# Kernel tuning notes

Measured on AMD Instinct MI355X. Metric: run time of the kernel, lower is better.

## Reference

```python
import jax, jax.numpy as jnp
import numpy as np

TAU, LBDA, THETA = 0.25, 0.15, 0.3
N_WARPS, N_ITERS = 1, 30
EPS = 1e-12  # GRAD_IS_ZERO

GAUSS = jnp.array([
    [0.000874, 0.006976, 0.01386, 0.006976, 0.000874],
    [0.006976, 0.0557, 0.110656, 0.0557, 0.006976],
    [0.01386, 0.110656, 0.219833, 0.110656, 0.01386],
    [0.006976, 0.0557, 0.110656, 0.0557, 0.006976],
    [0.000874, 0.006976, 0.01386, 0.006976, 0.000874]], dtype=jnp.float32)


def to_gray(x):  # [B,3,H,W] -> [B,1,H,W], BGR-style weights from repo
    w = jnp.array([0.114, 0.587, 0.299], x.dtype)
    return jnp.einsum('bchw,c->bhw', x, w)[:, None]


def normalize_pair(x1, x2):
    mn = jnp.minimum(x1.min(), x2.min())
    mx = jnp.maximum(x1.max(), x2.max())
    den = mx - mn
    return 255.0 * (x1 - mn) / den, 255.0 * (x2 - mn) / den


def gaussian_smooth(x):
    k = GAUSS[None, None].astype(x.dtype)
    return jax.lax.conv_general_dilated(x, k, (1, 1), 'SAME')


def centered_grad(x):  # central differences, one-sided at borders (scaled 0.5)
    dx = jnp.concatenate([0.5 * (x[..., 1:2] - x[..., 0:1]),
                          0.5 * (x[..., 2:] - x[..., :-2]),
                          0.5 * (x[..., -1:] - x[..., -2:-1])], axis=-1)
    dy = jnp.concatenate([0.5 * (x[..., 1:2, :] - x[..., 0:1, :]),
                          0.5 * (x[..., 2:, :] - x[..., :-2, :]),
                          0.5 * (x[..., -1:, :] - x[..., -2:-1, :])], axis=-2)
    return dx, dy


def fwd_grad(x):  # forward differences, zero at last col/row
    dx = jnp.concatenate([x[..., 1:] - x[..., :-1], jnp.zeros_like(x[..., :1])], axis=-1)
    dy = jnp.concatenate([x[..., 1:, :] - x[..., :-1, :], jnp.zeros_like(x[..., :1, :])], axis=-2)
    return dx, dy


def divergence(px, py):  # adjoint of fwd_grad (backward differences with boundary handling)
    xp = jnp.concatenate([jnp.zeros_like(px[..., :1]), px[..., :-1]], axis=-1)
    yp = jnp.concatenate([jnp.zeros_like(py[..., :1, :]), py[..., :-1, :]], axis=-2)
    dx = jnp.concatenate([xp[..., 1:] - xp[..., :-1], -xp[..., -1:]], axis=-1)
    dy = jnp.concatenate([yp[..., 1:, :] - yp[..., :-1, :], -yp[..., -1:, :]], axis=-2)
    return dx + dy


def warp(x, u, v):  # grid_sample bilinear, align_corners=True, zeros padding
    B, C, H, W = x.shape
    base_x = jnp.linspace(-1.0, 1.0, W)[None, None, :]
    base_y = jnp.linspace(-1.0, 1.0, H)[None, :, None]
    gx = base_x + 2.0 * u[:, 0] / W   # [B,H,W]
    gy = base_y + 2.0 * v[:, 0] / H
    ix = (gx + 1.0) * 0.5 * (W - 1)
    iy = (gy + 1.0) * 0.5 * (H - 1)
    ix0 = jnp.floor(ix); iy0 = jnp.floor(iy)
    wx = ix - ix0; wy = iy - iy0

    def gather(yy, xx):
        valid = (xx >= 0) & (xx <= W - 1) & (yy >= 0) & (yy <= H - 1)
        xi = jnp.clip(xx, 0, W - 1).astype(jnp.int32)
        yi = jnp.clip(yy, 0, H - 1).astype(jnp.int32)
        flat = (yi * W + xi).reshape(B, 1, H * W)
        g = jnp.take_along_axis(x.reshape(B, C, H * W), flat, axis=2).reshape(B, C, H, W)
        return g * valid[:, None].astype(x.dtype)

    return (gather(iy0, ix0) * ((1 - wx) * (1 - wy))[:, None]
            + gather(iy0, ix0 + 1) * (wx * (1 - wy))[:, None]
            + gather(iy0 + 1, ix0) * ((1 - wx) * wy)[:, None]
            + gather(iy0 + 1, ix0 + 1) * (wx * wy)[:, None])


def tvnet_scale(x1, x2, u1, u2):
    l_t = LBDA * THETA
    taut = TAU / THETA
    d2x, d2y = centered_grad(x2)
    p11 = jnp.zeros_like(x1); p12 = jnp.zeros_like(x1)
    p21 = jnp.zeros_like(x1); p22 = jnp.zeros_like(x1)
    rho = jnp.zeros_like(x1)
    for _ in range(N_WARPS):
        x2w = warp(x2, u1, u2)
        dxw = warp(d2x, u1, u2)
        dyw = warp(d2y, u1, u2)
        grad = dxw ** 2 + dyw ** 2 + EPS
        rho_c = x2w - dxw * u1 - dyw * u2 - x1

        def body(carry, _):
            u1, u2, p11, p12, p21, p22, _ = carry
            rho = rho_c + dxw * u1 + dyw * u2 + EPS
            th = l_t * grad
            m3 = (rho >= -th) & (rho <= th) & (grad > EPS)
            coef = (jnp.where(rho < -th, l_t, 0.0)
                    + jnp.where(rho > th, -l_t, 0.0)
                    + jnp.where(m3, -rho / grad, 0.0))
            v1 = coef * dxw + u1
            v2 = coef * dyw + u2
            u1n = v1 + THETA * divergence(p11, p12)
            u2n = v2 + THETA * divergence(p21, p22)
            u1x, u1y = fwd_grad(u1n)
            u2x, u2y = fwd_grad(u2n)
            ng1 = 1.0 + taut * jnp.sqrt(u1x ** 2 + u1y ** 2 + EPS)
            ng2 = 1.0 + taut * jnp.sqrt(u2x ** 2 + u2y ** 2 + EPS)
            p11n = (p11 + taut * u1x) / ng1
            p12n = (p12 + taut * u1y) / ng1
            p21n = (p21 + taut * u2x) / ng2
            p22n = (p22 + taut * u2y) / ng2
            return (u1n, u2n, p11n, p12n, p21n, p22n, rho), None

        (u1, u2, p11, p12, p21, p22, rho), _ = jax.lax.scan(
            body, (u1, u2, p11, p12, p21, p22, rho), None, length=N_ITERS)
    return u1, u2, rho


def setup_inputs() -> dict:
    key = jax.random.key(0)
    k1, k2 = jax.random.split(key)
    x1 = jax.random.uniform(k1, (8, 3, 256, 256), dtype=jnp.float32)
    x2 = jax.random.uniform(k2, (8, 3, 256, 256), dtype=jnp.float32)
    return {"x1": x1, "x2": x2}


def reference(x1, x2):
    g1 = to_gray(x1)
    g2 = to_gray(x2)
    n1, n2 = normalize_pair(g1, g2)
    s1 = gaussian_smooth(n1)
    s2 = gaussian_smooth(n2)
    u1 = jnp.zeros_like(s1)
    u2 = jnp.zeros_like(s1)
    u1, u2, rho = tvnet_scale(s1, s2, u1, u2)
    return jnp.concatenate([u1, u2, rho], axis=1)  # [B,3,H,W]
```

## Files before the change

### kernel.cpp

```cpp
#include <hip/hip_runtime.h>
#include <hip/hip_fp16.h>
#include <math.h>

typedef float v2f __attribute__((ext_vector_type(2)));
static __device__ __forceinline__ v2f v2(float a, float b){ v2f r; r.x=a; r.y=b; return r; }
#define PKFMA(a,b,c) __builtin_elementwise_fma((a),(b),(c))

#define HH 256
#define WW 256
#define BB 8
#define NPIX (BB*HH*WW)
#define HWPLANE (HH*WW)
#define EPSF 1e-12f

#define TS 32
#define HL 10
#define SS (TS + 2*HL)
#define SS2 (SS*SS)
#define NTH 1024
#define NPAIR 2048
#define NSING (SS2 - NPAIR)
#define OWNBIT (1<<13)

#define GSS (TS + 6)
#define GSS2 (GSS*GSS)
#define S2S (TS + 2)
#define S2S2 (S2S*S2S)

constexpr float L_T   = (float)(0.15*0.3);
constexpr float TAUT  = (float)(0.25/0.3);
constexpr float THETA = 0.3f;

static __device__ __constant__ float GK[25] = {
  0.000874f, 0.006976f, 0.01386f,  0.006976f, 0.000874f,
  0.006976f, 0.0557f,   0.110656f, 0.0557f,   0.006976f,
  0.01386f,  0.110656f, 0.219833f, 0.110656f, 0.01386f,
  0.006976f, 0.0557f,   0.110656f, 0.0557f,   0.006976f,
  0.000874f, 0.006976f, 0.01386f,  0.006976f, 0.000874f };


__global__ void k_gray_minmax(const float* __restrict__ x1, const float* __restrict__ x2,
                              float* __restrict__ g1, float* __restrict__ g2,
                              unsigned int* __restrict__ mnmx) {
    __shared__ float smn[4], smx[4];
    float mn = 1e30f, mx = -1e30f;
    int stride = gridDim.x * blockDim.x;
    const int NV = 2*NPIX/4;
    for (int v = blockIdx.x*blockDim.x + threadIdx.x; v < NV; v += stride) {
        int img = v >> 17;
        int rem = v & (NPIX/4 - 1);
        const float* x = img ? x2 : x1;
        float* g = img ? g2 : g1;
        int b = rem >> 14;
        int pix = (rem & (HWPLANE/4 - 1)) << 2;
        const float* base = x + (size_t)b*3*HWPLANE + pix;
        float4 c0 = *(const float4*)(base);
        float4 c1 = *(const float4*)(base + HWPLANE);
        float4 c2 = *(const float4*)(base + 2*HWPLANE);
        float4 gr;
        gr.x = 0.114f*c0.x + 0.587f*c1.x + 0.299f*c2.x;
        gr.y = 0.114f*c0.y + 0.587f*c1.y + 0.299f*c2.y;
        gr.z = 0.114f*c0.z + 0.587f*c1.z + 0.299f*c2.z;
        gr.w = 0.114f*c0.w + 0.587f*c1.w + 0.299f*c2.w;
        *(float4*)(g + ((size_t)rem << 2)) = gr;
        mn = fminf(mn, fminf(fminf(gr.x, gr.y), fminf(gr.z, gr.w)));
        mx = fmaxf(mx, fmaxf(fmaxf(gr.x, gr.y), fmaxf(gr.z, gr.w)));
    }
    #pragma unroll
    for (int off = 32; off; off >>= 1) {
        mn = fminf(mn, __shfl_down(mn, off, 64));
        mx = fmaxf(mx, __shfl_down(mx, off, 64));
    }
    int wid = threadIdx.x >> 6;
    if ((threadIdx.x & 63) == 0) { smn[wid] = mn; smx[wid] = mx; }
    __syncthreads();
    if (threadIdx.x == 0) {
        mn = fminf(fminf(smn[0], smn[1]), fminf(smn[2], smn[3]));
        mx = fmaxf(fmaxf(smx[0], smx[1]), fmaxf(smx[2], smx[3]));
        atomicMin(&mnmx[0], __float_as_uint(mn));
        atomicMax((int*)&mnmx[1], (int)__float_as_uint(mx));
    }
}

__global__ void __launch_bounds__(256)
k_smooth_grad(const float* __restrict__ g1, const float* __restrict__ g2,
              const unsigned int* __restrict__ mnmx, float4* __restrict__ dxr) {
    __shared__ float gn1[GSS2], gn2[GSS2], s2L[S2S2];
    const int blk   = blockIdx.x;
    const int plane = blk >> 6;
    const int t     = blk & 63;
    const int oy0   = (t >> 3) << 5;
    const int ox0   = (t & 7) << 5;
    const int pbse  = plane * HWPLANE;
    const int tid   = threadIdx.x;

    const float mn  = __uint_as_float(mnmx[0]);
    const float inv = 255.0f / (__uint_as_float(mnmx[1]) - mn);

    for (int s = tid; s < GSS2; s += 256) {
        int sy = s / GSS, sx = s - sy*GSS;
        int gy = oy0 - 3 + sy, gx = ox0 - 3 + sx;
        bool im = (gx >= 0) & (gx < WW) & (gy >= 0) & (gy < HH);
        int gi = pbse + gy*WW + gx;
        gn1[s] = im ? (g1[gi] - mn)*inv : 0.f;
        gn2[s] = im ? (g2[gi] - mn)*inv : 0.f;
    }
    __syncthreads();

    for (int c = tid; c < S2S2; c += 256) {
        int sy = c / S2S, sx = c - sy*S2S;
        const float* gb = gn2 + sy*GSS + sx;
        float acc = 0.f;
        #pragma unroll
        for (int i = 0; i < 5; ++i)
            #pragma unroll
            for (int j = 0; j < 5; ++j)
                acc += gb[i*GSS + j] * GK[i*5 + j];
        s2L[c] = acc;
    }
    float s1r[4];
    #pragma unroll
    for (int i = 0; i < 4; ++i) {
        int c = tid + i*256;
        int oy = c >> 5, ox = c & 31;
        const float* gb = gn1 + (oy+1)*GSS + (ox+1);
        float acc = 0.f;
        #pragma unroll
        for (int ii = 0; ii < 5; ++ii)
            #pragma unroll
            for (int jj = 0; jj < 5; ++jj)
                acc += gb[ii*GSS + jj] * GK[ii*5 + jj];
        s1r[i] = acc;
    }
    __syncthreads();

    #pragma unroll
    for (int i = 0; i < 4; ++i) {
        int c = tid + i*256;
        int oy = c >> 5, ox = c & 31;
        int gy = oy0 + oy, gx = ox0 + ox;
        int sc = (oy+1)*S2S + (ox+1);
        float s2c = s2L[sc];
        float xp = (gx < WW-1) ? s2L[sc+1]    : s2c;
        float xm = (gx > 0)    ? s2L[sc-1]    : s2c;
        float yp = (gy < HH-1) ? s2L[sc+S2S]  : s2c;
        float ym = (gy > 0)    ? s2L[sc-S2S]  : s2c;
        float dx = 0.5f*(xp - xm), dy = 0.5f*(yp - ym);
        float grad = fmaf(dx, dx, fmaf(dy, dy, EPSF));
        float rgr  = __builtin_amdgcn_rcpf(grad);
        dxr[pbse + gy*WW + gx] = make_float4(dx, dy, s2c - s1r[i], rgr);
    }
}

__global__ void __launch_bounds__(NTH)
k_iter10(float* __restrict__ F, float* __restrict__ out, int itbase) {
    const float4* DXR = (const float4*)F;
    const int j  = itbase / HL;
    const int rd = j & 1;
    const uint4* Xr = (const uint4*)(F + (size_t)NPIX*(rd ? 12 : 6));
    uint4*       Xw = (uint4*)(F + (size_t)NPIX*(rd ? 6 : 12));

    __shared__ v2f u12[SS2];
    __shared__ v2f pa [SS2];
    __shared__ v2f pb [SS2];

    const int blk   = blockIdx.x;
    const int plane = blk >> 6;
    const int t     = blk & 63;
    const int gy0   = ((t >> 3) << 5) - HL;
    const int gx0   = ((t & 7) << 5) - HL;
    const int pbse  = plane * HWPLANE;
    const int tid   = threadIdx.x;
    const int sxmax = WW-1 - gx0;
    const int symax = HH-1 - gy0;

    int ccP, ccS;
    v2f dv[3]; float rcv[3], rgr[3];
    v2f ru[3], rpa[3], rpb[3];

    {
        int ku0=0,ku1=0,ku2=0, kp0=0,kp1=0,kp2=0, ow0=0,ow2=0;
        #pragma unroll
        for (int i = 0; i < 3; ++i) {
            dv[i]=v2(0.f,0.f); rcv[i]=EPSF; rgr[i]=0.f;
            ru[i]=v2(0.f,0.f); rpa[i]=v2(0.f,0.f); rpb[i]=v2(0.f,0.f);
            if (i == 2 && tid >= NSING) continue;
            int s = (i < 2) ? (2*tid + i) : (NPAIR + tid);
            int sy = s / SS, sx = s - sy*SS;
            int gy = gy0 + sy, gx = gx0 + sx;
            bool im = (gx >= 0) & (gx < WW) & (gy >= 0) & (gy < HH);
            if (im) {
                int m  = min(min(sy-1, sx-1), min(SS-1-sy, SS-1-sx));
                int mp = min(m, min(SS-2-sy, SS-2-sx));
                int ku = max(m,  -1) + 1;
                int kp = max(mp, -1) + 1;
                int ow = (int)((sy >= HL) & (sy < HL+TS) & (sx >= HL) & (sx < HL+TS));
                if (i == 0) { ku0=ku; kp0=kp; ow0=ow; }
                else if (i == 1) { ku1=ku; kp1=kp; ow0|=ow; }
                else { ku2=ku; kp2=kp; ow2=ow; }
                int gi = pbse + gy*WW + gx;
                float4 dvv = DXR[gi];
                dv[i] = v2(dvv.x, dvv.y); rcv[i] = dvv.z + EPSF; rgr[i] = dvv.w;
                if (itbase) {
                    uint4 xv = Xr[gi];
                    float2 uf = __half22float2(*(__half2*)&xv.x);
                    float2 af = __half22float2(*(__half2*)&xv.y);
                    float2 bf = __half22float2(*(__half2*)&xv.z);
                    ru[i]=v2(uf.x,uf.y); rpa[i]=v2(af.x,af.y); rpb[i]=v2(bf.x,bf.y);
                }
            }
        }
        int s0 = 2*tid, sy0 = s0 / SS, sx0 = s0 - sy0*SS;
        ccP = (max(kp0,kp1) << 24) | (max(ku0,ku1) << 16)
            | (ow0 ? OWNBIT : 0) | (sy0 << 6) | sx0;
        if (tid < NSING) {
            int s2 = NPAIR + tid, sy2 = s2 / SS, sx2 = s2 - sy2*SS;
            ccS = (kp2 << 24) | (ku2 << 16) | (ow2 ? OWNBIT : 0) | (sy2 << 6) | sx2;
        } else ccS = 0;
        *(float4*)&u12[s0] = make_float4(ru[0].x,ru[0].y,ru[1].x,ru[1].y);
        *(float4*)&pa [s0] = make_float4(rpa[0].x,rpa[0].y,rpa[1].x,rpa[1].y);
        *(float4*)&pb [s0] = make_float4(rpb[0].x,rpb[0].y,rpb[1].x,rpb[1].y);
        if (tid < NSING) {
            int s2 = NPAIR + tid;
            u12[s2]=ru[2]; pa[s2]=rpa[2]; pb[s2]=rpb[2];
        }
    }
    __syncthreads();

    #pragma unroll 1
    for (int k = 0; k < HL; ++k) {
        const bool lastk = (k == HL-1);
        const bool it29  = (itbase + k == 29);

        if (k < ((ccP >> 16) & 0xFF)) {
            int s0 = 2*tid;
            v2f pal0 = pa[s0-1];
            float4 pb2 = *(const float4*)&pb[s0-SS];
            float rho0 = fmaf(dv[0].x, ru[0].x, fmaf(dv[0].y, ru[0].y, rcv[0]));
            float rho1 = fmaf(dv[1].x, ru[1].x, fmaf(dv[1].y, ru[1].y, rcv[1]));
            float co0 = fminf(fmaxf(-rho0 * rgr[0], -L_T), L_T);
            float co1 = fminf(fmaxf(-rho1 * rgr[1], -L_T), L_T);
            v2f d0 = (rpa[0] - pal0)   + (rpb[0] - v2(pb2.x,pb2.y));
            v2f d1 = (rpa[1] - rpa[0]) + (rpb[1] - v2(pb2.z,pb2.w));
            v2f un0 = PKFMA(v2(THETA,THETA), d0, PKFMA(v2(co0,co0), dv[0], ru[0]));
            v2f un1 = PKFMA(v2(THETA,THETA), d1, PKFMA(v2(co1,co1), dv[1], ru[1]));
            if (it29) {
                if (ccP & OWNBIT) {
                    int sy = (ccP >> 6) & 63, sx = ccP & 63;
                    float2* o = (float2*)(out + (size_t)plane*3*HWPLANE + (gy0+sy)*WW + (gx0+sx));
                    o[0]         = make_float2(un0.x, un1.x);
                    o[HWPLANE/2] = make_float2(un0.y, un1.y);
                    o[HWPLANE]   = make_float2(rho0, rho1);
                }
            } else {
                ru[0] = un0; ru[1] = un1;
                *(float4*)&u12[s0] = make_float4(un0.x,un0.y,un1.x,un1.y);
            }
        }
        if (k < ((ccS >> 16) & 0xFF)) {
            int s = NPAIR + tid;
            float rho = fmaf(dv[2].x, ru[2].x, fmaf(dv[2].y, ru[2].y, rcv[2]));
            float co  = fminf(fmaxf(-rho * rgr[2], -L_T), L_T);
            v2f pal = pa[s-1], pbu = pb[s-SS];
            v2f d  = (rpa[2] - pal) + (rpb[2] - pbu);
            v2f un = PKFMA(v2(THETA,THETA), d, PKFMA(v2(co,co), dv[2], ru[2]));
            if (it29) {
                if (ccS & OWNBIT) {
                    int sy = (ccS >> 6) & 63, sx = ccS & 63;
                    float* o = out + (size_t)plane*3*HWPLANE + (gy0+sy)*WW + (gx0+sx);
                    o[0] = un.x; o[HWPLANE] = un.y; o[2*HWPLANE] = rho;
                }
            } else {
                ru[2] = un;
                u12[s] = un;
            }
        }
        if (it29) return;
        __syncthreads();

        if (k < (int)((unsigned)ccP >> 24)) {
            int s0 = 2*tid;
            int sy = (ccP >> 6) & 63, sx = ccP & 63;
            float fdm  = (sy     < symax) ? 1.f : 0.f;
            float fbm0 = (sx     < sxmax) ? 1.f : 0.f;
            float fbm1 = (sx + 1 < sxmax) ? 1.f : 0.f;
            v2f ur1 = u12[s0+2];
            float4 ud2 = *(const float4*)&u12[s0+SS];
            v2f ux0 = (ru[1] - ru[0]) * fbm0;
            v2f uy0 = (v2(ud2.x,ud2.y) - ru[0]) * fdm;
            v2f ux1 = (ur1 - ru[1]) * fbm1;
            v2f uy1 = (v2(ud2.z,ud2.w) - ru[1]) * fdm;
            v2f q0 = PKFMA(ux0, ux0, PKFMA(uy0, uy0, v2(EPSF,EPSF)));
            v2f q1 = PKFMA(ux1, ux1, PKFMA(uy1, uy1, v2(EPSF,EPSF)));
            v2f ng0 = PKFMA(v2(TAUT,TAUT), v2(__builtin_amdgcn_sqrtf(q0.x),__builtin_amdgcn_sqrtf(q0.y)), v2(1.f,1.f));
            v2f ng1 = PKFMA(v2(TAUT,TAUT), v2(__builtin_amdgcn_sqrtf(q1.x),__builtin_amdgcn_sqrtf(q1.y)), v2(1.f,1.f));
            v2f r0 = v2(__builtin_amdgcn_rcpf(ng0.x), __builtin_amdgcn_rcpf(ng0.y));
            v2f r1 = v2(__builtin_amdgcn_rcpf(ng1.x), __builtin_amdgcn_rcpf(ng1.y));
            rpa[0] = PKFMA(v2(TAUT,TAUT), ux0, rpa[0]) * r0;
            rpb[0] = PKFMA(v2(TAUT,TAUT), uy0, rpb[0]) * r0;
            rpa[1] = PKFMA(v2(TAUT,TAUT), ux1, rpa[1]) * r1;
            rpb[1] = PKFMA(v2(TAUT,TAUT), uy1, rpb[1]) * r1;
            if (!lastk) {
                *(float4*)&pa[s0] = make_float4(rpa[0].x,rpa[0].y,rpa[1].x,rpa[1].y);
                *(float4*)&pb[s0] = make_float4(rpb[0].x,rpb[0].y,rpb[1].x,rpb[1].y);
            } else if (ccP & OWNBIT) {
                int gi = pbse + (gy0+sy)*WW + (gx0+sx);
                __half2 h0u = __floats2half2_rn(ru[0].x, ru[0].y);
                __half2 h0a = __floats2half2_rn(rpa[0].x, rpa[0].y);
                __half2 h0b = __floats2half2_rn(rpb[0].x, rpb[0].y);
                __half2 h1u = __floats2half2_rn(ru[1].x, ru[1].y);
                __half2 h1a = __floats2half2_rn(rpa[1].x, rpa[1].y);
                __half2 h1b = __floats2half2_rn(rpb[1].x, rpb[1].y);
                uint4 x0, x1;
                x0.x = *(unsigned int*)&h0u; x0.y = *(unsigned int*)&h0a;
                x0.z = *(unsigned int*)&h0b; x0.w = 0u;
                x1.x = *(unsigned int*)&h1u; x1.y = *(unsigned int*)&h1a;
                x1.z = *(unsigned int*)&h1b; x1.w = 0u;
                Xw[gi]   = x0;
                Xw[gi+1] = x1;
            }
        }
        if (k < (int)((unsigned)ccS >> 24)) {
            int s = NPAIR + tid;
            int sy = (ccS >> 6) & 63, sx = ccS & 63;
            float fbm = (sx < sxmax) ? 1.f : 0.f;
            float fdm = (sy < symax) ? 1.f : 0.f;
            v2f ux = (u12[s+1]  - ru[2]) * fbm;
            v2f uy = (u12[s+SS] - ru[2]) * fdm;
            v2f q  = PKFMA(ux, ux, PKFMA(uy, uy, v2(EPSF,EPSF)));
            v2f ng = PKFMA(v2(TAUT,TAUT), v2(__builtin_amdgcn_sqrtf(q.x),__builtin_amdgcn_sqrtf(q.y)), v2(1.f,1.f));
            v2f r  = v2(__builtin_amdgcn_rcpf(ng.x), __builtin_amdgcn_rcpf(ng.y));
            rpa[2] = PKFMA(v2(TAUT,TAUT), ux, rpa[2]) * r;
            rpb[2] = PKFMA(v2(TAUT,TAUT), uy, rpb[2]) * r;
            if (!lastk) {
                pa[s] = rpa[2];
                pb[s] = rpb[2];
            } else if (ccS & OWNBIT) {
                int gi = pbse + (gy0+sy)*WW + (gx0+sx);
                __half2 hu = __floats2half2_rn(ru[2].x, ru[2].y);
                __half2 ha = __floats2half2_rn(rpa[2].x, rpa[2].y);
                __half2 hb = __floats2half2_rn(rpb[2].x, rpb[2].y);
                uint4 xv;
                xv.x = *(unsigned int*)&hu; xv.y = *(unsigned int*)&ha;
                xv.z = *(unsigned int*)&hb; xv.w = 0u;
                Xw[gi] = xv;
            }
        }
        if (!lastk) __syncthreads();
    }
}

extern "C" void kernel_launch(void* const* d_in, const int* in_sizes, int n_in,
                              void* d_out, int out_size, void* d_ws, size_t ws_size,
                              hipStream_t stream) {
    const float* x1 = (const float*)d_in[0];
    const float* x2 = (const float*)d_in[1];
    float* out = (float*)d_out;

    char* ws = (char*)d_ws;
    unsigned int* mnmx = (unsigned int*)ws;
    float* F = (float*)(ws + 256);
    float4* dxr = (float4*)F;
    float*  g1  = F + 4*(size_t)NPIX;
    float*  g2  = F + 5*(size_t)NPIX;

    k_gray_minmax<<<dim3(512), dim3(256), 0, stream>>>(x1, x2, g1, g2, mnmx);
    k_smooth_grad<<<dim3(512), dim3(256), 0, stream>>>(g1, g2, mnmx, dxr);

    for (int itbase = 0; itbase < 30; itbase += HL)
        k_iter10<<<dim3(512), dim3(NTH), 0, stream>>>(F, out, itbase);
}
```

Before: 164.2 us.

## Fuse three iteration launches into a persistent kernel with grid barriers

Replaces the three k_iter10 launches with one k_iter30 kernel. It runs all 30 iterations in three blocks of ten and uses a global atomic counter as a grid-wide barrier between blocks. After each barrier, owned pixels keep their fp32 state in registers and only halo pixels are reloaded from the fp16 exchange buffer, which removes launch gaps and some global traffic. This relies on all 512 blocks being co-resident, or the barrier deadlocks. The added launch-bounds occupancy hint may also force register spills.

```diff
diff --git a/kernel.cpp b/kernel.cpp
--- a/kernel.cpp
+++ b/kernel.cpp
@@ -21,6 +21,7 @@
 #define NPAIR 2048
 #define NSING (SS2 - NPAIR)
 #define OWNBIT (1<<13)
+#define NBLK 512
 
 #define GSS (TS + 6)
 #define GSS2 (GSS*GSS)
@@ -43,6 +44,7 @@
                               float* __restrict__ g1, float* __restrict__ g2,
                               unsigned int* __restrict__ mnmx) {
     __shared__ float smn[4], smx[4];
+    if (blockIdx.x == 0 && threadIdx.x == 0) { mnmx[8] = 0u; mnmx[9] = 0u; }
     float mn = 1e30f, mx = -1e30f;
     int stride = gridDim.x * blockDim.x;
     const int NV = 2*NPIX/4;
@@ -152,13 +154,10 @@
     }
 }
 
-__global__ void __launch_bounds__(NTH)
-k_iter10(float* __restrict__ F, float* __restrict__ out, int itbase) {
+__global__ void __launch_bounds__(NTH, 8)
+k_iter30(float* __restrict__ F, float* __restrict__ out,
+         unsigned int* __restrict__ bar) {
     const float4* DXR = (const float4*)F;
-    const int j  = itbase / HL;
-    const int rd = j & 1;
-    const uint4* Xr = (const uint4*)(F + (size_t)NPIX*(rd ? 12 : 6));
-    uint4*       Xw = (uint4*)(F + (size_t)NPIX*(rd ? 6 : 12));
 
     __shared__ v2f u12[SS2];
     __shared__ v2f pa [SS2];
@@ -201,13 +200,6 @@
                 int gi = pbse + gy*WW + gx;
                 float4 dvv = DXR[gi];
                 dv[i] = v2(dvv.x, dvv.y); rcv[i] = dvv.z + EPSF; rgr[i] = dvv.w;
-                if (itbase) {
-                    uint4 xv = Xr[gi];
-                    float2 uf = __half22float2(*(__half2*)&xv.x);
-                    float2 af = __half22float2(*(__half2*)&xv.y);
-                    float2 bf = __half22float2(*(__half2*)&xv.z);
-                    ru[i]=v2(uf.x,uf.y); rpa[i]=v2(af.x,af.y); rpb[i]=v2(bf.x,bf.y);
-                }
             }
         }
         int s0 = 2*tid, sy0 = s0 / SS, sx0 = s0 - sy0*SS;
@@ -217,136 +209,186 @@
             int s2 = NPAIR + tid, sy2 = s2 / SS, sx2 = s2 - sy2*SS;
             ccS = (kp2 << 24) | (ku2 << 16) | (ow2 ? OWNBIT : 0) | (sy2 << 6) | sx2;
         } else ccS = 0;
-        *(float4*)&u12[s0] = make_float4(ru[0].x,ru[0].y,ru[1].x,ru[1].y);
-        *(float4*)&pa [s0] = make_float4(rpa[0].x,rpa[0].y,rpa[1].x,rpa[1].y);
-        *(float4*)&pb [s0] = make_float4(rpb[0].x,rpb[0].y,rpb[1].x,rpb[1].y);
+        *(float4*)&u12[s0] = make_float4(0.f,0.f,0.f,0.f);
+        *(float4*)&pa [s0] = make_float4(0.f,0.f,0.f,0.f);
+        *(float4*)&pb [s0] = make_float4(0.f,0.f,0.f,0.f);
         if (tid < NSING) {
             int s2 = NPAIR + tid;
-            u12[s2]=ru[2]; pa[s2]=rpa[2]; pb[s2]=rpb[2];
+            u12[s2]=v2(0.f,0.f); pa[s2]=v2(0.f,0.f); pb[s2]=v2(0.f,0.f);
         }
     }
     __syncthreads();
 
     #pragma unroll 1
-    for (int k = 0; k < HL; ++k) {
-        const bool lastk = (k == HL-1);
-        const bool it29  = (itbase + k == 29);
-
-        if (k < ((ccP >> 16) & 0xFF)) {
-            int s0 = 2*tid;
-            v2f pal0 = pa[s0-1];
-            float4 pb2 = *(const float4*)&pb[s0-SS];
-            float rho0 = fmaf(dv[0].x, ru[0].x, fmaf(dv[0].y, ru[0].y, rcv[0]));
-            float rho1 = fmaf(dv[1].x, ru[1].x, fmaf(dv[1].y, ru[1].y, rcv[1]));
-            float co0 = fminf(fmaxf(-rho0 * rgr[0], -L_T), L_T);
-            float co1 = fminf(fmaxf(-rho1 * rgr[1], -L_T), L_T);
-            v2f d0 = (rpa[0] - pal0)   + (rpb[0] - v2(pb2.x,pb2.y));
-            v2f d1 = (rpa[1] - rpa[0]) + (rpb[1] - v2(pb2.z,pb2.w));
-            v2f un0 = PKFMA(v2(THETA,THETA), d0, PKFMA(v2(co0,co0), dv[0], ru[0]));
-            v2f un1 = PKFMA(v2(THETA,THETA), d1, PKFMA(v2(co1,co1), dv[1], ru[1]));
-            if (it29) {
-                if (ccP & OWNBIT) {
-                    int sy = (ccP >> 6) & 63, sx = ccP & 63;
-                    float2* o = (float2*)(out + (size_t)plane*3*HWPLANE + (gy0+sy)*WW + (gx0+sx));
-                    o[0]         = make_float2(un0.x, un1.x);
-                    o[HWPLANE/2] = make_float2(un0.y, un1.y);
-                    o[HWPLANE]   = make_float2(rho0, rho1);
+    for (int j = 0; j < 3; ++j) {
+        uint4* Xj = (uint4*)(F + (size_t)NPIX*(j == 0 ? 6 : 12));
+
+        #pragma unroll 1
+        for (int k = 0; k < HL; ++k) {
+            const bool lastk = (k == HL-1);
+            const bool it29  = (j == 2) && lastk;
+
+            if (k < ((ccP >> 16) & 0xFF)) {
+                int s0 = 2*tid;
+                v2f pal0 = pa[s0-1];
+                float4 pb2 = *(const float4*)&pb[s0-SS];
+                float rho0 = fmaf(dv[0].x, ru[0].x, fmaf(dv[0].y, ru[0].y, rcv[0]));
+                float rho1 = fmaf(dv[1].x, ru[1].x, fmaf(dv[1].y, ru[1].y, rcv[1]));
+                float co0 = fminf(fmaxf(-rho0 * rgr[0], -L_T), L_T);
+                float co1 = fminf(fmaxf(-rho1 * rgr[1], -L_T), L_T);
+                v2f d0 = (rpa[0] - pal0)   + (rpb[0] - v2(pb2.x,pb2.y));
+                v2f d1 = (rpa[1] - rpa[0]) + (rpb[1] - v2(pb2.z,pb2.w));
+                v2f un0 = PKFMA(v2(THETA,THETA), d0, PKFMA(v2(co0,co0), dv[0], ru[0]));
+                v2f un1 = PKFMA(v2(THETA,THETA), d1, PKFMA(v2(co1,co1), dv[1], ru[1]));
+                if (it29) {
+                    if (ccP & OWNBIT) {
+                        int sy = (ccP >> 6) & 63, sx = ccP & 63;
+                        float2* o = (float2*)(out + (size_t)plane*3*HWPLANE + (gy0+sy)*WW + (gx0+sx));
+                        o[0]         = make_float2(un0.x, un1.x);
+                        o[HWPLANE/2] = make_float2(un0.y, un1.y);
+                        o[HWPLANE]   = make_float2(rho0, rho1);
+                    }
+                } else {
+                    ru[0] = un0; ru[1] = un1;
+                    *(float4*)&u12[s0] = make_float4(un0.x,un0.y,un1.x,un1.y);
                 }
-            } else {
-                ru[0] = un0; ru[1] = un1;
-                *(float4*)&u12[s0] = make_float4(un0.x,un0.y,un1.x,un1.y);
-            }
-        }
-        if (k < ((ccS >> 16) & 0xFF)) {
-            int s = NPAIR + tid;
-            float rho = fmaf(dv[2].x, ru[2].x, fmaf(dv[2].y, ru[2].y, rcv[2]));
-            float co  = fminf(fmaxf(-rho * rgr[2], -L_T), L_T);
-            v2f pal = pa[s-1], pbu = pb[s-SS];
-            v2f d  = (rpa[2] - pal) + (rpb[2] - pbu);
-            v2f un = PKFMA(v2(THETA,THETA), d, PKFMA(v2(co,co), dv[2], ru[2]));
-            if (it29) {
-                if (ccS & OWNBIT) {
-                    int sy = (ccS >> 6) & 63, sx = ccS & 63;
-                    float* o = out + (size_t)plane*3*HWPLANE + (gy0+sy)*WW + (gx0+sx);
-                    o[0] = un.x; o[HWPLANE] = un.y; o[2*HWPLANE] = rho;
+            }
+            if (k < ((ccS >> 16) & 0xFF)) {
+                int s = NPAIR + tid;
+                float rho = fmaf(dv[2].x, ru[2].x, fmaf(dv[2].y, ru[2].y, rcv[2]));
+                float co  = fminf(fmaxf(-rho * rgr[2], -L_T), L_T);
+                v2f pal = pa[s-1], pbu = pb[s-SS];
+                v2f d  = (rpa[2] - pal) + (rpb[2] - pbu);
+                v2f un = PKFMA(v2(THETA,THETA), d, PKFMA(v2(co,co), dv[2], ru[2]));
+                if (it29) {
+                    if (ccS & OWNBIT) {
+                        int sy = (ccS >> 6) & 63, sx = ccS & 63;
+                        float* o = out + (size_t)plane*3*HWPLANE + (gy0+sy)*WW + (gx0+sx);
+                        o[0] = un.x; o[HWPLANE] = un.y; o[2*HWPLANE] = rho;
+                    }
+                } else {
+                    ru[2] = un;
+                    u12[s] = un;
                 }
-            } else {
-                ru[2] = un;
-                u12[s] = un;
-            }
-        }
-        if (it29) return;
-        __syncthreads();
-
-        if (k < (int)((unsigned)ccP >> 24)) {
-            int s0 = 2*tid;
-            int sy = (ccP >> 6) & 63, sx = ccP & 63;
-            float fdm  = (sy     < symax) ? 1.f : 0.f;
-            float fbm0 = (sx     < sxmax) ? 1.f : 0.f;
-            float fbm1 = (sx + 1 < sxmax) ? 1.f : 0.f;
-            v2f ur1 = u12[s0+2];
-            float4 ud2 = *(const float4*)&u12[s0+SS];
-            v2f ux0 = (ru[1] - ru[0]) * fbm0;
-            v2f uy0 = (v2(ud2.x,ud2.y) - ru[0]) * fdm;
-            v2f ux1 = (ur1 - ru[1]) * fbm1;
-            v2f uy1 = (v2(ud2.z,ud2.w) - ru[1]) * fdm;
-            v2f q0 = PKFMA(ux0, ux0, PKFMA(uy0, uy0, v2(EPSF,EPSF)));
-            v2f q1 = PKFMA(ux1, ux1, PKFMA(uy1, uy1, v2(EPSF,EPSF)));
-            v2f ng0 = PKFMA(v2(TAUT,TAUT), v2(__builtin_amdgcn_sqrtf(q0.x),__builtin_amdgcn_sqrtf(q0.y)), v2(1.f,1.f));
-            v2f ng1 = PKFMA(v2(TAUT,TAUT), v2(__builtin_amdgcn_sqrtf(q1.x),__builtin_amdgcn_sqrtf(q1.y)), v2(1.f,1.f));
-            v2f r0 = v2(__builtin_amdgcn_rcpf(ng0.x), __builtin_amdgcn_rcpf(ng0.y));
-            v2f r1 = v2(__builtin_amdgcn_rcpf(ng1.x), __builtin_amdgcn_rcpf(ng1.y));
-            rpa[0] = PKFMA(v2(TAUT,TAUT), ux0, rpa[0]) * r0;
-            rpb[0] = PKFMA(v2(TAUT,TAUT), uy0, rpb[0]) * r0;
-            rpa[1] = PKFMA(v2(TAUT,TAUT), ux1, rpa[1]) * r1;
-            rpb[1] = PKFMA(v2(TAUT,TAUT), uy1, rpb[1]) * r1;
-            if (!lastk) {
+            }
+            if (it29) return;
+            __syncthreads();
+
+            if (k < (int)((unsigned)ccP >> 24)) {
+                int s0 = 2*tid;
+                int sy = (ccP >> 6) & 63, sx = ccP & 63;
+                float fdm  = (sy     < symax) ? 1.f : 0.f;
+                float fbm0 = (sx     < sxmax) ? 1.f : 0.f;
+                float fbm1 = (sx + 1 < sxmax) ? 1.f : 0.f;
+                v2f ur1 = u12[s0+2];
+                float4 ud2 = *(const float4*)&u12[s0+SS];
+                v2f ux0 = (ru[1] - ru[0]) * fbm0;
+                v2f uy0 = (v2(ud2.x,ud2.y) - ru[0]) * fdm;
+                v2f ux1 = (ur1 - ru[1]) * fbm1;
+                v2f uy1 = (v2(ud2.z,ud2.w) - ru[1]) * fdm;
+                v2f q0 = PKFMA(ux0, ux0, PKFMA(uy0, uy0, v2(EPSF,EPSF)));
+                v2f q1 = PKFMA(ux1, ux1, PKFMA(uy1, uy1, v2(EPSF,EPSF)));
+                v2f ng0 = PKFMA(v2(TAUT,TAUT), v2(__builtin_amdgcn_sqrtf(q0.x),__builtin_amdgcn_sqrtf(q0.y)), v2(1.f,1.f));
+                v2f ng1 = PKFMA(v2(TAUT,TAUT), v2(__builtin_amdgcn_sqrtf(q1.x),__builtin_amdgcn_sqrtf(q1.y)), v2(1.f,1.f));
+                v2f r0 = v2(__builtin_amdgcn_rcpf(ng0.x), __builtin_amdgcn_rcpf(ng0.y));
+                v2f r1 = v2(__builtin_amdgcn_rcpf(ng1.x), __builtin_amdgcn_rcpf(ng1.y));
+                rpa[0] = PKFMA(v2(TAUT,TAUT), ux0, rpa[0]) * r0;
+                rpb[0] = PKFMA(v2(TAUT,TAUT), uy0, rpb[0]) * r0;
+                rpa[1] = PKFMA(v2(TAUT,TAUT), ux1, rpa[1]) * r1;
+                rpb[1] = PKFMA(v2(TAUT,TAUT), uy1, rpb[1]) * r1;
                 *(float4*)&pa[s0] = make_float4(rpa[0].x,rpa[0].y,rpa[1].x,rpa[1].y);
                 *(float4*)&pb[s0] = make_float4(rpb[0].x,rpb[0].y,rpb[1].x,rpb[1].y);
-            } else if (ccP & OWNBIT) {
-                int gi = pbse + (gy0+sy)*WW + (gx0+sx);
-                __half2 h0u = __floats2half2_rn(ru[0].x, ru[0].y);
-                __half2 h0a = __floats2half2_rn(rpa[0].x, rpa[0].y);
-                __half2 h0b = __floats2half2_rn(rpb[0].x, rpb[0].y);
-                __half2 h1u = __floats2half2_rn(ru[1].x, ru[1].y);
-                __half2 h1a = __floats2half2_rn(rpa[1].x, rpa[1].y);
-                __half2 h1b = __floats2half2_rn(rpb[1].x, rpb[1].y);
-                uint4 x0, x1;
-                x0.x = *(unsigned int*)&h0u; x0.y = *(unsigned int*)&h0a;
-                x0.z = *(unsigned int*)&h0b; x0.w = 0u;
-                x1.x = *(unsigned int*)&h1u; x1.y = *(unsigned int*)&h1a;
-                x1.z = *(unsigned int*)&h1b; x1.w = 0u;
-                Xw[gi]   = x0;
-                Xw[gi+1] = x1;
-            }
-        }
-        if (k < (int)((unsigned)ccS >> 24)) {
-            int s = NPAIR + tid;
-            int sy = (ccS >> 6) & 63, sx = ccS & 63;
-            float fbm = (sx < sxmax) ? 1.f : 0.f;
-            float fdm = (sy < symax) ? 1.f : 0.f;
-            v2f ux = (u12[s+1]  - ru[2]) * fbm;
-            v2f uy = (u12[s+SS] - ru[2]) * fdm;
-            v2f q  = PKFMA(ux, ux, PKFMA(uy, uy, v2(EPSF,EPSF)));
-            v2f ng = PKFMA(v2(TAUT,TAUT), v2(__builtin_amdgcn_sqrtf(q.x),__builtin_amdgcn_sqrtf(q.y)), v2(1.f,1.f));
-            v2f r  = v2(__builtin_amdgcn_rcpf(ng.x), __builtin_amdgcn_rcpf(ng.y));
-            rpa[2] = PKFMA(v2(TAUT,TAUT), ux, rpa[2]) * r;
-            rpb[2] = PKFMA(v2(TAUT,TAUT), uy, rpb[2]) * r;
-            if (!lastk) {
+                if (lastk && (ccP & OWNBIT)) {
+                    int gi = pbse + (gy0+sy)*WW + (gx0+sx);
+                    __half2 h0u = __floats2half2_rn(ru[0].x, ru[0].y);
+                    __half2 h0a = __floats2half2_rn(rpa[0].x, rpa[0].y);
+                    __half2 h0b = __floats2half2_rn(rpb[0].x, rpb[0].y);
+                    __half2 h1u = __floats2half2_rn(ru[1].x, ru[1].y);
+                    __half2 h1a = __floats2half2_rn(rpa[1].x, rpa[1].y);
+                    __half2 h1b = __floats2half2_rn(rpb[1].x, rpb[1].y);
+                    uint4 x0, x1;
+                    x0.x = *(unsigned int*)&h0u; x0.y = *(unsigned int*)&h0a;
+                    x0.z = *(unsigned int*)&h0b; x0.w = 0u;
+                    x1.x = *(unsigned int*)&h1u; x1.y = *(unsigned int*)&h1a;
+                    x1.z = *(unsigned int*)&h1b; x1.w = 0u;
+                    Xj[gi]   = x0;
+                    Xj[gi+1] = x1;
+                }
+            }
+            if (k < (int)((unsigned)ccS >> 24)) {
+                int s = NPAIR + tid;
+                int sy = (ccS >> 6) & 63, sx = ccS & 63;
+                float fbm = (sx < sxmax) ? 1.f : 0.f;
+                float fdm = (sy < symax) ? 1.f : 0.f;
+                v2f ux = (u12[s+1]  - ru[2]) * fbm;
+                v2f uy = (u12[s+SS] - ru[2]) * fdm;
+                v2f q  = PKFMA(ux, ux, PKFMA(uy, uy, v2(EPSF,EPSF)));
+                v2f ng = PKFMA(v2(TAUT,TAUT), v2(__builtin_amdgcn_sqrtf(q.x),__builtin_amdgcn_sqrtf(q.y)), v2(1.f,1.f));
+                v2f r  = v2(__builtin_amdgcn_rcpf(ng.x), __builtin_amdgcn_rcpf(ng.y));
+                rpa[2] = PKFMA(v2(TAUT,TAUT), ux, rpa[2]) * r;
+                rpb[2] = PKFMA(v2(TAUT,TAUT), uy, rpb[2]) * r;
                 pa[s] = rpa[2];
                 pb[s] = rpb[2];
-            } else if (ccS & OWNBIT) {
-                int gi = pbse + (gy0+sy)*WW + (gx0+sx);
-                __half2 hu = __floats2half2_rn(ru[2].x, ru[2].y);
-                __half2 ha = __floats2half2_rn(rpa[2].x, rpa[2].y);
-                __half2 hb = __floats2half2_rn(rpb[2].x, rpb[2].y);
-                uint4 xv;
-                xv.x = *(unsigned int*)&hu; xv.y = *(unsigned int*)&ha;
-                xv.z = *(unsigned int*)&hb; xv.w = 0u;
-                Xw[gi] = xv;
-            }
-        }
-        if (!lastk) __syncthreads();
+                if (lastk && (ccS & OWNBIT)) {
+                    int gi = pbse + (gy0+sy)*WW + (gx0+sx);
+                    __half2 hu = __floats2half2_rn(ru[2].x, ru[2].y);
+                    __half2 ha = __floats2half2_rn(rpa[2].x, rpa[2].y);
+                    __half2 hb = __floats2half2_rn(rpb[2].x, rpb[2].y);
+                    uint4 xv;
+                    xv.x = *(unsigned int*)&hu; xv.y = *(unsigned int*)&ha;
+                    xv.z = *(unsigned int*)&hb; xv.w = 0u;
+                    Xj[gi] = xv;
+                }
+            }
+            __syncthreads();
+        }
+
+        if (tid == 0) {
+            __threadfence();
+            __hip_atomic_fetch_add(&bar[j], 1u, __ATOMIC_RELEASE, __HIP_MEMORY_SCOPE_AGENT);
+            while (__hip_atomic_load(&bar[j], __ATOMIC_ACQUIRE, __HIP_MEMORY_SCOPE_AGENT) < (unsigned)NBLK)
+                __builtin_amdgcn_s_sleep(16);
+            __threadfence();
+        }
+        __syncthreads();
+
+        {
+            int sy = (ccP >> 6) & 63, sx = ccP & 63;
+            int gy = gy0 + sy, gx = gx0 + sx;
+            bool im = (gx >= 0) & (gx < WW) & (gy >= 0) & (gy < HH);
+            if (im && !(ccP & OWNBIT)) {
+                int gi = pbse + gy*WW + gx;
+                uint4 x0 = Xj[gi], x1 = Xj[gi+1];
+                float2 u0 = __half22float2(*(__half2*)&x0.x);
+                float2 a0 = __half22float2(*(__half2*)&x0.y);
+                float2 b0 = __half22float2(*(__half2*)&x0.z);
+                float2 u1 = __half22float2(*(__half2*)&x1.x);
+                float2 a1 = __half22float2(*(__half2*)&x1.y);
+                float2 b1 = __half22float2(*(__half2*)&x1.z);
+                ru[0]=v2(u0.x,u0.y); rpa[0]=v2(a0.x,a0.y); rpb[0]=v2(b0.x,b0.y);
+                ru[1]=v2(u1.x,u1.y); rpa[1]=v2(a1.x,a1.y); rpb[1]=v2(b1.x,b1.y);
+                int s0 = 2*tid;
+                *(float4*)&u12[s0] = make_float4(u0.x,u0.y,u1.x,u1.y);
+                *(float4*)&pa [s0] = make_float4(a0.x,a0.y,a1.x,a1.y);
+                *(float4*)&pb [s0] = make_float4(b0.x,b0.y,b1.x,b1.y);
+            }
+        }
+        if (tid < NSING) {
+            int sy = (ccS >> 6) & 63, sx = ccS & 63;
+            int gy = gy0 + sy, gx = gx0 + sx;
+            bool im = (gx >= 0) & (gx < WW) & (gy >= 0) & (gy < HH);
+            if (im && !(ccS & OWNBIT)) {
+                int gi = pbse + gy*WW + gx;
+                uint4 xv = Xj[gi];
+                float2 uf = __half22float2(*(__half2*)&xv.x);
+                float2 af = __half22float2(*(__half2*)&xv.y);
+                float2 bf = __half22float2(*(__half2*)&xv.z);
+                ru[2]=v2(uf.x,uf.y); rpa[2]=v2(af.x,af.y); rpb[2]=v2(bf.x,bf.y);
+                int s2 = NPAIR + tid;
+                u12[s2]=ru[2]; pa[s2]=rpa[2]; pb[s2]=rpb[2];
+            }
+        }
+        __syncthreads();
     }
 }
 
@@ -366,7 +408,5 @@
 
     k_gray_minmax<<<dim3(512), dim3(256), 0, stream>>>(x1, x2, g1, g2, mnmx);
     k_smooth_grad<<<dim3(512), dim3(256), 0, stream>>>(g1, g2, mnmx, dxr);
-
-    for (int itbase = 0; itbase < 30; itbase += HL)
-        k_iter10<<<dim3(512), dim3(NTH), 0, stream>>>(F, out, itbase);
+    k_iter30<<<dim3(NBLK), dim3(NTH), 0, stream>>>(F, out, mnmx + 8);
 }
```

After: 435.5 us. 2.65x slower.
